# Optimization experiments

Measured on AMD Instinct MI355X. Metric: run time of the kernel, lower is better.

## Reference

```python
import jax, jax.numpy as jnp
import numpy as np

DIM = 1024      # main_dim
HEADS = 16      # attn_num
HEAD = DIM // HEADS
S = 1024        # seq len per half
BH = 1          # batch per half (x_input batch = 2*BH)
PE = 16; FE = 16      # experts per group
PD = 512; FD = 512    # expert hidden dims
DS = 2048             # shared_expert_dim
K = 4                 # top_k routed experts
EPS = 1e-5
THETA = 10000.0
SCALE_P = 1.0; SCALE_F = 1.0


def rmsnorm(x, w, eps=EPS):
    return x * jax.lax.rsqrt(jnp.mean(x * x, -1, keepdims=True) + eps) * w


def rope(x, theta=THETA):
    # x: [b, h, s, a]; matches RotaryEmb: y1 = x1*cos + x2*sin, y2 = -x1*sin + x2*cos
    a = x.shape[-1]; s = x.shape[2]
    inv = (1.0 / theta) ** (jnp.arange(0, a, 2, dtype=jnp.float32) / a)
    fr = jnp.arange(s, dtype=jnp.float32)[:, None] * inv[None, :]   # [s, a//2]
    cos, sin = jnp.cos(fr), jnp.sin(fr)
    x1, x2 = jnp.split(x, 2, -1)
    return jnp.concatenate([x1 * cos + x2 * sin, -x1 * sin + x2 * cos], -1)


def moe(xt, block, idx, sc):
    # xt: [T, d]; block: [3, E, d, f] (gate/up/down SwiGLU); idx, sc: [T, K]
    g = jnp.einsum('td,edf->tef', xt, block[0])
    u = jnp.einsum('td,edf->tef', xt, block[1])
    h = jax.nn.silu(g) * u
    out_all = jnp.einsum('tef,edf->ted', h, block[2])        # per-expert outputs
    sel = jnp.take_along_axis(out_all, idx[:, :, None], 1)   # [T, K, d]
    return jnp.sum(sel * sc[:, :, None], 1)


def setup_inputs():
    key = jax.random.key(0)
    ks = jax.random.split(key, 16)
    w = 0.02  # param scale for numerical sanity
    d = {}
    d['x_input'] = jax.random.normal(ks[0], (2 * BH, S, DIM), jnp.float32)
    d['p_indices'] = jax.random.randint(ks[1], (BH * S, K), 0, PE)
    d['p_values'] = jax.random.normal(ks[2], (BH * S, K), jnp.float32)
    d['f_indices'] = jax.random.randint(ks[3], (BH * S, K), 0, FE)
    d['f_values'] = jax.random.normal(ks[4], (BH * S, K), jnp.float32)
    d['attn_norm_w'] = jnp.ones((DIM,), jnp.float32)
    d['ffn_norm_w'] = jnp.ones((DIM,), jnp.float32)
    d['W_attn'] = jax.random.normal(ks[5], (DIM, 3 * DIM), jnp.float32) * w
    d['W_attn_o'] = jax.random.normal(ks[6], (DIM, DIM), jnp.float32) * w
    d['ffn_up_w'] = jax.random.normal(ks[7], (DIM, 2 * DS), jnp.float32) * w
    d['ffn_down_w'] = jax.random.normal(ks[8], (DS, DIM), jnp.float32) * w
    d['p_ffn_experts'] = jax.random.normal(ks[9], (3, PE, DIM, PD), jnp.float32) * w
    d['f_ffn_experts'] = jax.random.normal(ks[10], (3, FE, DIM, FD), jnp.float32) * w
    d['p_token_keys'] = jax.random.normal(ks[11], (DIM, PE), jnp.float32) * w
    d['f_token_keys'] = jax.random.normal(ks[12], (DIM, FE), jnp.float32) * w
    d['p_router_bias'] = jnp.zeros((PE,), jnp.float32)
    d['f_router_bias'] = jnp.zeros((FE,), jnp.float32)
    return d


def reference(x_input, p_indices, p_values, f_indices, f_values,
              attn_norm_w, ffn_norm_w, W_attn, W_attn_o, ffn_up_w, ffn_down_w,
              p_ffn_experts, f_ffn_experts, p_token_keys, f_token_keys,
              p_router_bias, f_router_bias):
    B2, s, dim = x_input.shape
    b = B2 // 2
    # attention block
    x = rmsnorm(x_input, attn_norm_w)
    xq, xk, xv = jnp.split(x @ W_attn, 3, -1)
    heads = lambda t: t.reshape(B2, s, HEADS, HEAD).transpose(0, 2, 1, 3)
    xq, xk, xv = heads(xq), heads(xk), heads(xv)
    xq, xk = rope(xq), rope(xk)
    # dual interleave: '(c b) h s a -> b h (s c) a', c=2
    il = lambda t: t.reshape(2, b, HEADS, s, HEAD).transpose(1, 2, 3, 0, 4).reshape(b, HEADS, 2 * s, HEAD)
    q, k, v = il(xq), il(xk), il(xv)
    scores = jnp.einsum('bhqa,bhka->bhqk', q, k) / jnp.sqrt(jnp.float32(HEAD))
    causal = jnp.tril(jnp.ones((2 * s, 2 * s), bool))
    attn = jax.nn.softmax(jnp.where(causal, scores, -jnp.inf), -1)
    o = jnp.einsum('bhqk,bhka->bhqa', attn, v)
    # de-interleave: 'b h (s c) a -> (c b) s (h a)'
    o = o.reshape(b, HEADS, s, 2, HEAD).transpose(3, 0, 2, 1, 4).reshape(B2, s, dim)
    x_ffn_input = o @ W_attn_o + x_input
    x_ffn = rmsnorm(x_ffn_input, ffn_norm_w)
    p_x = x_ffn[:b].reshape(-1, dim)
    f_x = x_ffn[b:].reshape(-1, dim)
    # router: token keys + bias, sigmoid, normalize
    p_vals = p_values + jnp.take_along_axis(p_x @ p_token_keys, p_indices, -1) + p_router_bias[p_indices]
    f_vals = f_values + jnp.take_along_axis(f_x @ f_token_keys, f_indices, -1) + f_router_bias[f_indices]
    p_sc = jax.nn.sigmoid(p_vals)
    p_sc = p_sc / jnp.sum(p_sc, -1, keepdims=True) * SCALE_P
    f_sc = jax.nn.sigmoid(f_vals)
    f_sc = f_sc / jnp.sum(f_sc, -1, keepdims=True) * SCALE_F
    py = moe(p_x, p_ffn_experts, p_indices, p_sc).reshape(b, s, dim)
    fy = moe(f_x, f_ffn_experts, f_indices, f_sc).reshape(b, s, dim)
    y = jnp.concatenate([py, fy], 0) + x_ffn_input
    # shared expert (SwiGLU)
    x1, x2 = jnp.split(x_ffn @ ffn_up_w, 2, -1)
    y = y + (jax.nn.silu(x1) * x2) @ ffn_down_w
    return y
```

## Files before the change

### kernel.cpp

```cpp
#include <hip/hip_runtime.h>


#define T_TOT   2048
#define DMODEL  1024
#define NHEADS  16
#define NEXP    16
#define FDIM    512
#define DSH     2048
#define NPAIR   8192

typedef __attribute__((ext_vector_type(4))) float          f32x4;
typedef __attribute__((ext_vector_type(8))) short          s16x8;
typedef __attribute__((ext_vector_type(8))) unsigned short u16x8;
typedef __attribute__((ext_vector_type(2))) unsigned int   u32x2;

__device__ __forceinline__ float sigm(float x) { return 1.0f / (1.0f + __expf(-x)); }

__device__ __forceinline__ unsigned short bf16r(float f) {
    union { float f; unsigned int u; } v; v.f = f;
    unsigned int r = v.u + 0x7fffu + ((v.u >> 16) & 1u);
    return (unsigned short)(r >> 16);
}

__device__ __forceinline__ unsigned int cvtpk(float lo, float hi) {
    unsigned int r;
    asm("v_cvt_pk_bf16_f32 %0, %1, %2" : "=v"(r) : "v"(lo), "v"(hi));
    return r;
}

__device__ __forceinline__ float ubf(unsigned short u) {
    union { unsigned int i; float f; } v; v.i = (unsigned int)u << 16; return v.f;
}

__device__ __forceinline__ int pair2tok(int p) {
    return ((p >> 12) << 10) + ((p & 4095) >> 2);
}

template<int NI>
__device__ __forceinline__ void tile_mma(
        const unsigned short (*Asb)[40], const unsigned short (*Bsb)[40],
        int wm, int wn, int lr, int lk, f32x4 (&acc)[4][NI]) {
    s16x8 af[4], bfr[NI];
    #pragma unroll
    for (int mi = 0; mi < 4; ++mi)
        af[mi] = *(const s16x8*)&Asb[wm + mi * 16 + lr][lk];
    #pragma unroll
    for (int ni = 0; ni < NI; ++ni)
        bfr[ni] = *(const s16x8*)&Bsb[wn + ni * 16 + lr][lk];
    #pragma unroll
    for (int mi = 0; mi < 4; ++mi)
        #pragma unroll
        for (int ni = 0; ni < NI; ++ni)
            acc[mi][ni] = __builtin_amdgcn_mfma_f32_16x16x32_bf16(
                              af[mi], bfr[ni], acc[mi][ni], 0, 0, 0);
}

__device__ __forceinline__ void gu_mma(
        const unsigned short (*Asb)[40], const unsigned short (*Bg)[40],
        const unsigned short (*Bu)[40], int wm, int wn, int lr, int lk,
        f32x4 (&ag)[4][2], f32x4 (&au)[4][2]) {
    s16x8 af[4], bg[2], bu[2];
    #pragma unroll
    for (int mi = 0; mi < 4; ++mi)
        af[mi] = *(const s16x8*)&Asb[wm + mi * 16 + lr][lk];
    #pragma unroll
    for (int ni = 0; ni < 2; ++ni) {
        bg[ni] = *(const s16x8*)&Bg[wn + ni * 16 + lr][lk];
        bu[ni] = *(const s16x8*)&Bu[wn + ni * 16 + lr][lk];
    }
    #pragma unroll
    for (int mi = 0; mi < 4; ++mi)
        #pragma unroll
        for (int ni = 0; ni < 2; ++ni) {
            ag[mi][ni] = __builtin_amdgcn_mfma_f32_16x16x32_bf16(
                             af[mi], bg[ni], ag[mi][ni], 0, 0, 0);
            au[mi][ni] = __builtin_amdgcn_mfma_f32_16x16x32_bf16(
                             af[mi], bu[ni], au[mi][ni], 0, 0, 0);
        }
}

__global__ void rmsnorm_kernel(const float* __restrict__ x,
                               const float* __restrict__ w,
                               unsigned short* __restrict__ out) {
    int t = blockIdx.x, tid = threadIdx.x;
    float4 xv = *(const float4*)(x + (size_t)t * DMODEL + tid * 4);
    __shared__ float rb[256];
    rb[tid] = xv.x*xv.x + xv.y*xv.y + xv.z*xv.z + xv.w*xv.w;
    __syncthreads();
    for (int s = 128; s > 0; s >>= 1) { if (tid < s) rb[tid] += rb[tid+s]; __syncthreads(); }
    float scale = rsqrtf(rb[0] * (1.0f/1024.0f) + 1e-5f);
    float4 wv = *(const float4*)(w + tid * 4);
    u32x2 pv;
    pv.x = cvtpk(xv.x * scale * wv.x, xv.y * scale * wv.y);
    pv.y = cvtpk(xv.z * scale * wv.z, xv.w * scale * wv.w);
    *(u32x2*)(out + (size_t)t * DMODEL + tid * 4) = pv;
}

__global__ void rope_kernel(unsigned short* __restrict__ qkv) {
    int t = blockIdx.x, tid = threadIdx.x;
    int s = t & 1023;
    unsigned short* row = qkv + (size_t)t * 3072;
    for (int pp = tid; pp < 512; pp += 256) {
        int h = pp >> 5, i = pp & 31;
        float fr = (float)s * exp2f(-0.41524101186092028f * (float)i);
        float sn, cs;
        sincosf(fr, &sn, &cs);
        int o1 = (h << 6) + i, o2 = o1 + 32;
        float x1 = ubf(row[o1]), x2 = ubf(row[o2]);
        row[o1] = bf16r(x1 * cs + x2 * sn);
        row[o2] = bf16r(x2 * cs - x1 * sn);
        x1 = ubf(row[1024 + o1]); x2 = ubf(row[1024 + o2]);
        row[1024 + o1] = bf16r(x1 * cs + x2 * sn);
        row[1024 + o2] = bf16r(x2 * cs - x1 * sn);
    }
}

__global__ __launch_bounds__(256) void attn_mfma_kernel(
        const unsigned short* __restrict__ qkv,
        unsigned short* __restrict__ attn_out) {
    int qt = blockIdx.x, h = blockIdx.y;
    __shared__ alignas(16) unsigned short Qs[64][72];
    __shared__ alignas(16) unsigned short Ks[64][72];
    __shared__ alignas(16) unsigned short Vt[64][72];
    __shared__ alignas(16) unsigned short Ps[4][16][72];
    int tid = threadIdx.x;
    int w = tid >> 6, lane = tid & 63;
    int lr = lane & 15, lkg = lane >> 4, lk = lkg << 3;
    int kr = tid >> 3, kc = (tid & 7) << 3;

    #pragma unroll
    for (int i = 0; i < 2; ++i) {
        int rr = kr + 32 * i;
        int p = qt * 64 + rr;
        int t = ((p & 1) << 10) + (p >> 1);
        u16x8 q = *(const u16x8*)(qkv + (size_t)t * 3072 + (h << 6) + kc);
        unsigned int* dst = (unsigned int*)&Qs[rr][kc];
        dst[0] = cvtpk(ubf(q[0]) * 0.125f, ubf(q[1]) * 0.125f);
        dst[1] = cvtpk(ubf(q[2]) * 0.125f, ubf(q[3]) * 0.125f);
        dst[2] = cvtpk(ubf(q[4]) * 0.125f, ubf(q[5]) * 0.125f);
        dst[3] = cvtpk(ubf(q[6]) * 0.125f, ubf(q[7]) * 0.125f);
    }
    u16x8 pkv[2], pvv[2];
    #pragma unroll
    for (int i = 0; i < 2; ++i) {
        int rr = kr + 32 * i;
        int t = ((rr & 1) << 10) + (rr >> 1);
        const unsigned short* b = qkv + (size_t)t * 3072 + (h << 6) + kc;
        pkv[i] = *(const u16x8*)(b + 1024);
        pvv[i] = *(const u16x8*)(b + 2048);
    }
    __syncthreads();
    s16x8 qa0 = *(const s16x8*)&Qs[(w << 4) + lr][lk];
    s16x8 qa1 = *(const s16x8*)&Qs[(w << 4) + lr][32 + lk];

    float m[4], l[4];
    f32x4 oacc[4];
    #pragma unroll
    for (int r = 0; r < 4; ++r) { m[r] = -1e30f; l[r] = 0.0f; }
    #pragma unroll
    for (int df = 0; df < 4; ++df) oacc[df] = (f32x4)0.0f;

    int qrow_base = qt * 64 + w * 16 + lkg * 4;

    for (int kb = 0; kb <= qt; ++kb) {
        __syncthreads();
        u16x8 ck[2], cv[2];
        #pragma unroll
        for (int i = 0; i < 2; ++i) { ck[i] = pkv[i]; cv[i] = pvv[i]; }
        if (kb + 1 <= qt) {
            #pragma unroll
            for (int i = 0; i < 2; ++i) {
                int rr = kr + 32 * i;
                int p = (kb + 1) * 64 + rr;
                int t = ((p & 1) << 10) + (p >> 1);
                const unsigned short* b = qkv + (size_t)t * 3072 + (h << 6) + kc;
                pkv[i] = *(const u16x8*)(b + 1024);
                pvv[i] = *(const u16x8*)(b + 2048);
            }
        }
        #pragma unroll
        for (int i = 0; i < 2; ++i) {
            int rr = kr + 32 * i;
            *(u16x8*)&Ks[rr][kc] = ck[i];
            #pragma unroll
            for (int j = 0; j < 8; ++j) {
                int vrow = kc + j;
                int sw = ((vrow >> 3) & 7) << 3;
                Vt[vrow][rr ^ sw] = cv[i][j];
            }
        }
        __syncthreads();

        f32x4 s[4];
        #pragma unroll
        for (int nf = 0; nf < 4; ++nf) {
            s16x8 b0 = *(const s16x8*)&Ks[nf * 16 + lr][lk];
            s16x8 b1 = *(const s16x8*)&Ks[nf * 16 + lr][32 + lk];
            f32x4 z = (f32x4)0.0f;
            z = __builtin_amdgcn_mfma_f32_16x16x32_bf16(qa0, b0, z, 0, 0, 0);
            z = __builtin_amdgcn_mfma_f32_16x16x32_bf16(qa1, b1, z, 0, 0, 0);
            s[nf] = z;
        }
        if (kb == qt) {
            #pragma unroll
            for (int nf = 0; nf < 4; ++nf) {
                int kcol = kb * 64 + nf * 16 + lr;
                #pragma unroll
                for (int r = 0; r < 4; ++r)
                    if (kcol > qrow_base + r) s[nf][r] = -1e30f;
            }
        }
        float mloc[4];
        #pragma unroll
        for (int r = 0; r < 4; ++r)
            mloc[r] = fmaxf(fmaxf(s[0][r], s[1][r]), fmaxf(s[2][r], s[3][r]));
        #pragma unroll
        for (int r = 0; r < 4; ++r) {
            mloc[r] = fmaxf(mloc[r], __shfl_xor(mloc[r], 1));
            mloc[r] = fmaxf(mloc[r], __shfl_xor(mloc[r], 2));
            mloc[r] = fmaxf(mloc[r], __shfl_xor(mloc[r], 4));
            mloc[r] = fmaxf(mloc[r], __shfl_xor(mloc[r], 8));
        }
        float alpha[4], psum[4];
        #pragma unroll
        for (int r = 0; r < 4; ++r) {
            float mnew = fmaxf(m[r], mloc[r]);
            alpha[r] = __expf(m[r] - mnew);
            m[r] = mnew;
            psum[r] = 0.0f;
        }
        #pragma unroll
        for (int nf = 0; nf < 4; ++nf)
            #pragma unroll
            for (int r = 0; r < 4; ++r) {
                float pv2 = __expf(s[nf][r] - m[r]);
                s[nf][r] = pv2;
                psum[r] += pv2;
            }
        #pragma unroll
        for (int r = 0; r < 4; ++r) {
            psum[r] += __shfl_xor(psum[r], 1);
            psum[r] += __shfl_xor(psum[r], 2);
            psum[r] += __shfl_xor(psum[r], 4);
            psum[r] += __shfl_xor(psum[r], 8);
            l[r] = l[r] * alpha[r] + psum[r];
        }
        #pragma unroll
        for (int nf = 0; nf < 4; ++nf)
            #pragma unroll
            for (int r = 0; r < 4; ++r)
                Ps[w][lkg * 4 + r][nf * 16 + lr] = bf16r(s[nf][r]);
        #pragma unroll
        for (int df = 0; df < 4; ++df)
            #pragma unroll
            for (int r = 0; r < 4; ++r)
                oacc[df][r] *= alpha[r];
        s16x8 pa0 = *(const s16x8*)&Ps[w][lr][lk];
        s16x8 pa1 = *(const s16x8*)&Ps[w][lr][32 + lk];
        #pragma unroll
        for (int df = 0; df < 4; ++df) {
            int vr = df * 16 + lr;
            int sw = ((vr >> 3) & 7) << 3;
            s16x8 v0 = *(const s16x8*)&Vt[vr][lk ^ sw];
            s16x8 v1 = *(const s16x8*)&Vt[vr][(32 + lk) ^ sw];
            oacc[df] = __builtin_amdgcn_mfma_f32_16x16x32_bf16(pa0, v0, oacc[df], 0, 0, 0);
            oacc[df] = __builtin_amdgcn_mfma_f32_16x16x32_bf16(pa1, v1, oacc[df], 0, 0, 0);
        }
    }

    float invl[4];
    #pragma unroll
    for (int r = 0; r < 4; ++r) invl[r] = 1.0f / l[r];
    #pragma unroll
    for (int r = 0; r < 4; ++r) {
        int qrow = qrow_base + r;
        int t = ((qrow & 1) << 10) + (qrow >> 1);
        unsigned short* op = attn_out + (size_t)t * 1024 + (h << 6) + lr;
        #pragma unroll
        for (int df = 0; df < 4; ++df)
            op[df * 16] = bf16r(oacc[df][r] * invl[r]);
    }
}

__global__ void router_kernel(const unsigned short* __restrict__ xffn,
        const float* __restrict__ p_keys, const float* __restrict__ f_keys,
        const int* __restrict__ p_idx, const int* __restrict__ f_idx,
        const float* __restrict__ p_val, const float* __restrict__ f_val,
        const float* __restrict__ p_bias, const float* __restrict__ f_bias,
        float* __restrict__ sc) {
    int tl = blockIdx.x, hf = blockIdx.y;
    int t = hf * 1024 + tl;
    const float* keys = hf ? f_keys : p_keys;
    const int* idx    = hf ? f_idx  : p_idx;
    const float* val  = hf ? f_val  : p_val;
    const float* bias = hf ? f_bias : p_bias;
    int tid = threadIdx.x;
    float acc[16];
    #pragma unroll
    for (int e = 0; e < 16; ++e) acc[e] = 0.0f;
    const unsigned short* x = xffn + (size_t)t * DMODEL;
    for (int d = tid; d < 1024; d += 256) {
        float xd = ubf(x[d]);
        const float* kr = keys + d * 16;
        #pragma unroll
        for (int e4 = 0; e4 < 4; ++e4) {
            float4 kv = *(const float4*)(kr + e4 * 4);
            acc[e4*4+0] += xd * kv.x;
            acc[e4*4+1] += xd * kv.y;
            acc[e4*4+2] += xd * kv.z;
            acc[e4*4+3] += xd * kv.w;
        }
    }
    #pragma unroll
    for (int e = 0; e < 16; ++e) {
        float v = acc[e];
        v += __shfl_down(v, 32); v += __shfl_down(v, 16); v += __shfl_down(v, 8);
        v += __shfl_down(v, 4);  v += __shfl_down(v, 2);  v += __shfl_down(v, 1);
        acc[e] = v;
    }
    __shared__ float part[4][16];
    __shared__ float logit[16];
    __shared__ float sg[4];
    int wave = tid >> 6, ln = tid & 63;
    if (ln == 0) {
        #pragma unroll
        for (int e = 0; e < 16; ++e) part[wave][e] = acc[e];
    }
    __syncthreads();
    if (tid < 16) logit[tid] = part[0][tid] + part[1][tid] + part[2][tid] + part[3][tid];
    __syncthreads();
    if (tid < 4) {
        int ii = idx[tl * 4 + tid];
        float v = val[tl * 4 + tid] + logit[ii] + bias[ii];
        sg[tid] = 1.0f / (1.0f + expf(-v));
    }
    __syncthreads();
    if (tid < 4) {
        float ssum = sg[0] + sg[1] + sg[2] + sg[3];
        sc[t * 4 + tid] = sg[tid] / ssum;
    }
}

__global__ __launch_bounds__(1024) void buckets_kernel(
        const int* __restrict__ p_idx, const int* __restrict__ f_idx,
        int* __restrict__ counts, int* __restrict__ offsets,
        int* __restrict__ pair_p) {
    __shared__ int lcnt[32], loff[32], lcur[32];
    int tid = threadIdx.x;
    if (tid < 32) { lcnt[tid] = 0; lcur[tid] = 0; }
    __syncthreads();
    for (int p = tid; p < NPAIR; p += 1024) {
        int hf = p >> 12, rem = p & 4095;
        int e = (hf ? f_idx : p_idx)[rem];
        atomicAdd(&lcnt[(hf << 4) + e], 1);
    }
    __syncthreads();
    if (tid == 0) {
        int o = 0;
        for (int b = 0; b < 32; ++b) { loff[b] = o; o += lcnt[b]; }
    }
    __syncthreads();
    for (int p = tid; p < NPAIR; p += 1024) {
        int hf = p >> 12, rem = p & 4095;
        int e = (hf ? f_idx : p_idx)[rem];
        int b = (hf << 4) + e;
        int pos = atomicAdd(&lcur[b], 1);
        pair_p[loff[b] + pos] = p;
    }
    if (tid < 32) { counts[tid] = lcnt[tid]; offsets[tid] = loff[tid]; }
}

template<int MODE, int BN2, int OUTBF>
__global__ __launch_bounds__(256) void mfma_gemm(
        const unsigned short* __restrict__ A, const float* __restrict__ B,
        void* __restrict__ Cv, const float* __restrict__ resid,
        int M, int N, int K) {
    constexpr int NI = BN2 / 32;
    __shared__ alignas(16) unsigned short As[2][128][40];
    __shared__ alignas(16) unsigned short Bs[2][BN2][40];
    int tid = threadIdx.x;
    int m0 = blockIdx.y * 128, n0 = blockIdx.x * BN2;
    int w = tid >> 6, lane = tid & 63;
    int wm = (w >> 1) * 64, wn = (w & 1) * (BN2 / 2);
    int lr = lane & 15, lk = (lane >> 4) << 3;
    int ar = tid >> 2, ac = (tid & 3) << 3;
    int bn = (tid >> 3) << 2, bk = (tid & 7) << 2;
    bool bact = true;
    if (BN2 == 64) bact = (tid < 128);
    const unsigned short* Ap0 = A + (size_t)(m0 + ar) * K + ac;
    const unsigned short* Ap1 = Ap0 + (size_t)64 * K;
    const float* Bp = B + (size_t)bk * N + n0 + bn;

    f32x4 acc[4][NI] = {};
    u16x8 aA0, aA1, aB0, aB1;
    f32x4 bA[4], bB[4];

#define GM_LOAD(A0, A1, BV, KK) do {                                      \
        A0 = *(const u16x8*)(Ap0 + (KK));                                 \
        A1 = *(const u16x8*)(Ap1 + (KK));                                 \
        if (bact) {                                                       \
            const float* bp_ = Bp + (size_t)(KK) * N;                     \
            _Pragma("unroll")                                             \
            for (int j = 0; j < 4; ++j)                                   \
                BV[j] = *(const f32x4*)(bp_ + (size_t)j * N);             \
        }                                                                 \
    } while (0)

#define GM_WRITE(BUF, A0, A1, BV) do {                                    \
        *(u16x8*)&As[BUF][ar][ac] = A0;                                   \
        *(u16x8*)&As[BUF][ar + 64][ac] = A1;                              \
        if (bact) {                                                       \
            _Pragma("unroll")                                             \
            for (int jj = 0; jj < 4; ++jj) {                              \
                u32x2 pv_;                                                \
                pv_.x = cvtpk(BV[0][jj], BV[1][jj]);                      \
                pv_.y = cvtpk(BV[2][jj], BV[3][jj]);                      \
                *(u32x2*)&Bs[BUF][bn + jj][bk] = pv_;                     \
            }                                                             \
        }                                                                 \
    } while (0)

    GM_LOAD(aA0, aA1, bA, 0);
    GM_LOAD(aB0, aB1, bB, 32);
    GM_WRITE(0, aA0, aA1, bA);
    __syncthreads();
    for (int k0 = 0; k0 < K; k0 += 64) {
        if (k0 + 64 < K) GM_LOAD(aA0, aA1, bA, k0 + 64);
        tile_mma<NI>(As[0], Bs[0], wm, wn, lr, lk, acc);
        GM_WRITE(1, aB0, aB1, bB);
        __syncthreads();
        if (k0 + 96 < K) GM_LOAD(aB0, aB1, bB, k0 + 96);
        tile_mma<NI>(As[1], Bs[1], wm, wn, lr, lk, acc);
        if (k0 + 64 < K) GM_WRITE(0, aA0, aA1, bA);
        __syncthreads();
    }
#undef GM_LOAD
#undef GM_WRITE

    #pragma unroll
    for (int mi = 0; mi < 4; ++mi)
        #pragma unroll
        for (int r = 0; r < 4; ++r) {
            int row = m0 + wm + mi * 16 + ((lane >> 4) << 2) + r;
            size_t rb = (size_t)row * N + n0 + wn + lr;
            #pragma unroll
            for (int ni = 0; ni < NI; ++ni) {
                size_t off = rb + ni * 16;
                float v = acc[mi][ni][r];
                if constexpr (OUTBF) {
                    ((unsigned short*)Cv)[off] = bf16r(v);
                } else {
                    float* Cf = (float*)Cv;
                    if (MODE == 1) v += Cf[off];
                    if (MODE == 2) v += resid[off];
                    Cf[off] = v;
                }
            }
        }
}

template<int MOE>
__global__ __launch_bounds__(256) void mfma_gateup(
        const unsigned short* __restrict__ X, const float* __restrict__ Wp,
        const float* __restrict__ Wf, const int* __restrict__ pair_p,
        const int* __restrict__ counts, const int* __restrict__ offsets,
        unsigned short* __restrict__ Hout) {
    __shared__ alignas(16) unsigned short As[2][128][40];
    __shared__ alignas(16) unsigned short Bsg[2][64][40];
    __shared__ alignas(16) unsigned short Bsu[2][64][40];
    __shared__ int toks[128];
    int tid = threadIdx.x;
    int rem = 128, slot0 = 0, m0 = 0, n0, ldb;
    const float *Wg, *Wu;
    if (MOE) {
        int bucket = blockIdx.y;
        int cnt = counts[bucket];
        int tile0 = blockIdx.x * 128;
        if (tile0 >= cnt) return;
        n0 = blockIdx.z * 64;
        int e = bucket & 15;
        const float* base = (bucket >> 4) ? Wf : Wp;
        Wg = base + (size_t)e * (DMODEL * FDIM) + n0;
        Wu = base + (size_t)(NEXP + e) * (DMODEL * FDIM) + n0;
        ldb = FDIM;
        slot0 = offsets[bucket] + tile0;
        rem = cnt - tile0;
        if (tid < 128)
            toks[tid] = (tid < rem) ? pair2tok(pair_p[slot0 + tid]) : 0;
    } else {
        m0 = blockIdx.y * 128;
        n0 = blockIdx.x * 64;
        Wg = Wp + n0;
        Wu = Wp + DSH + n0;
        ldb = 2 * DSH;
    }
    int w = tid >> 6, lane = tid & 63;
    int wm = (w >> 1) * 64, wn = (w & 1) * 32;
    int lr = lane & 15, lk = (lane >> 4) << 3;
    int ar = tid >> 2, ac = (tid & 3) << 3;
    int t2 = tid & 127, wq = tid >> 7;
    int bn = (t2 >> 3) << 2, bk = (t2 & 7) << 2;
    const float* bsrc = wq ? Wu : Wg;
    if (MOE) __syncthreads();
    const unsigned short *Xp0, *Xp1;
    {
        int x0 = MOE ? toks[ar] : (m0 + ar);
        int x1 = MOE ? toks[ar + 64] : (m0 + ar + 64);
        Xp0 = X + (size_t)x0 * DMODEL + ac;
        Xp1 = X + (size_t)x1 * DMODEL + ac;
    }
    const float* Bp = bsrc + (size_t)bk * ldb + bn;
    f32x4 ag[4][2] = {}, au[4][2] = {};
    u16x8 aA0, aA1, aB0, aB1;
    f32x4 bA[4], bB[4];

#define GU_LOAD(A0, A1, BV, KK) do {                                      \
        A0 = *(const u16x8*)(Xp0 + (KK));                                 \
        A1 = *(const u16x8*)(Xp1 + (KK));                                 \
        {                                                                 \
            const float* bp_ = Bp + (size_t)(KK) * ldb;                   \
            _Pragma("unroll")                                             \
            for (int j = 0; j < 4; ++j)                                   \
                BV[j] = *(const f32x4*)(bp_ + (size_t)j * ldb);           \
        }                                                                 \
    } while (0)

#define GU_WRITE(BUF, A0, A1, BV) do {                                    \
        *(u16x8*)&As[BUF][ar][ac] = A0;                                   \
        *(u16x8*)&As[BUF][ar + 64][ac] = A1;                              \
        {                                                                 \
            unsigned short (*bl_)[40] = wq ? Bsu[BUF] : Bsg[BUF];         \
            _Pragma("unroll")                                             \
            for (int jj = 0; jj < 4; ++jj) {                              \
                u32x2 pv_;                                                \
                pv_.x = cvtpk(BV[0][jj], BV[1][jj]);                      \
                pv_.y = cvtpk(BV[2][jj], BV[3][jj]);                      \
                *(u32x2*)&bl_[bn + jj][bk] = pv_;                         \
            }                                                             \
        }                                                                 \
    } while (0)

    GU_LOAD(aA0, aA1, bA, 0);
    GU_LOAD(aB0, aB1, bB, 32);
    GU_WRITE(0, aA0, aA1, bA);
    __syncthreads();
    for (int k0 = 0; k0 < DMODEL; k0 += 64) {
        if (k0 + 64 < DMODEL) GU_LOAD(aA0, aA1, bA, k0 + 64);
        gu_mma(As[0], Bsg[0], Bsu[0], wm, wn, lr, lk, ag, au);
        GU_WRITE(1, aB0, aB1, bB);
        __syncthreads();
        if (k0 + 96 < DMODEL) GU_LOAD(aB0, aB1, bB, k0 + 96);
        gu_mma(As[1], Bsg[1], Bsu[1], wm, wn, lr, lk, ag, au);
        if (k0 + 64 < DMODEL) GU_WRITE(0, aA0, aA1, bA);
        __syncthreads();
    }
#undef GU_LOAD
#undef GU_WRITE

    #pragma unroll
    for (int mi = 0; mi < 4; ++mi)
        #pragma unroll
        for (int r = 0; r < 4; ++r) {
            int rloc = wm + mi * 16 + ((lane >> 4) << 2) + r;
            if (MOE && rloc >= rem) continue;
            size_t rowb = MOE ? (size_t)(slot0 + rloc) * FDIM
                              : (size_t)(m0 + rloc) * DSH;
            #pragma unroll
            for (int ni = 0; ni < 2; ++ni) {
                float g = ag[mi][ni][r], u = au[mi][ni][r];
                Hout[rowb + n0 + wn + ni * 16 + lr] = bf16r(g * sigm(g) * u);
            }
        }
}

__global__ __launch_bounds__(256) void mfma_moe_down(
        const unsigned short* __restrict__ h_pairs,
        const float* __restrict__ p_experts, const float* __restrict__ f_experts,
        const int* __restrict__ pair_p, const int* __restrict__ counts,
        const int* __restrict__ offsets, const float* __restrict__ sc,
        float* __restrict__ y) {
    __shared__ alignas(16) unsigned short As[2][128][40];
    __shared__ alignas(16) unsigned short Bs[2][128][40];
    __shared__ int   tokd[128];
    __shared__ float scd[128];
    int tid = threadIdx.x;
    int bucket = blockIdx.y;
    int cnt = counts[bucket];
    int tile0 = blockIdx.x * 128;
    if (tile0 >= cnt) return;
    int d0 = blockIdx.z * 128;
    int e = bucket & 15;
    const float* base = (bucket >> 4) ? f_experts : p_experts;
    const float* Wd = base + (size_t)(2 * NEXP + e) * (DMODEL * FDIM);
    int slot0 = offsets[bucket] + tile0;
    int rem = cnt - tile0;
    if (tid < 128) {
        int ok = tid < rem;
        int pr = ok ? pair_p[slot0 + tid] : 0;
        tokd[tid] = pair2tok(pr);
        scd[tid]  = ok ? sc[pr] : 0.0f;
    }
    int w = tid >> 6, lane = tid & 63;
    int wm = (w >> 1) * 64, wn = (w & 1) * 64;
    int lr = lane & 15, lk = (lane >> 4) << 3;
    int ar = tid >> 2, ac = (tid & 3) << 3;
    int br = tid >> 3, bc = (tid & 7) << 2;
    const unsigned short* Ap0 = h_pairs + (size_t)(slot0 + ar) * FDIM + ac;
    const unsigned short* Ap1 = Ap0 + (size_t)64 * FDIM;
    const float* Bp0 = Wd + (size_t)(d0 + br) * FDIM + bc;
    f32x4 acc[4][4] = {};
    u16x8 aA0, aA1, aB0, aB1;
    f32x4 bA[4], bB[4];

#define MD_LOAD(A0, A1, BV, KK) do {                                      \
        A0 = *(const u16x8*)(Ap0 + (KK));                                 \
        A1 = *(const u16x8*)(Ap1 + (KK));                                 \
        _Pragma("unroll")                                                 \
        for (int i = 0; i < 4; ++i)                                       \
            BV[i] = *(const f32x4*)(Bp0 + (size_t)(32 * i) * FDIM + (KK));\
    } while (0)

#define MD_WRITE(BUF, A0, A1, BV) do {                                    \
        *(u16x8*)&As[BUF][ar][ac] = A0;                                   \
        *(u16x8*)&As[BUF][ar + 64][ac] = A1;                              \
        _Pragma("unroll")                                                 \
        for (int i = 0; i < 4; ++i) {                                     \
            u32x2 pv_;                                                    \
            pv_.x = cvtpk(BV[i][0], BV[i][1]);                            \
            pv_.y = cvtpk(BV[i][2], BV[i][3]);                            \
            *(u32x2*)&Bs[BUF][br + 32 * i][bc] = pv_;                     \
        }                                                                 \
    } while (0)

    MD_LOAD(aA0, aA1, bA, 0);
    MD_LOAD(aB0, aB1, bB, 32);
    MD_WRITE(0, aA0, aA1, bA);
    __syncthreads();
    for (int k0 = 0; k0 < FDIM; k0 += 64) {
        if (k0 + 64 < FDIM) MD_LOAD(aA0, aA1, bA, k0 + 64);
        tile_mma<4>(As[0], Bs[0], wm, wn, lr, lk, acc);
        MD_WRITE(1, aB0, aB1, bB);
        __syncthreads();
        if (k0 + 96 < FDIM) MD_LOAD(aB0, aB1, bB, k0 + 96);
        tile_mma<4>(As[1], Bs[1], wm, wn, lr, lk, acc);
        if (k0 + 64 < FDIM) MD_WRITE(0, aA0, aA1, bA);
        __syncthreads();
    }
#undef MD_LOAD
#undef MD_WRITE

    #pragma unroll
    for (int mi = 0; mi < 4; ++mi)
        #pragma unroll
        for (int r = 0; r < 4; ++r) {
            int rloc = wm + mi * 16 + ((lane >> 4) << 2) + r;
            if (rloc < rem) {
                int   t = tokd[rloc];
                float s = scd[rloc];
                float* yp = y + (size_t)t * DMODEL + d0 + wn + lr;
                #pragma unroll
                for (int ni = 0; ni < 4; ++ni)
                    atomicAdd(yp + ni * 16, s * acc[mi][ni][r]);
            }
        }
}

extern "C" void kernel_launch(void* const* d_in, const int* in_sizes, int n_in,
                              void* d_out, int out_size, void* d_ws, size_t ws_size,
                              hipStream_t stream) {
    const float* x_input  = (const float*)d_in[0];
    const int*   p_idx    = (const int*)d_in[1];
    const float* p_val    = (const float*)d_in[2];
    const int*   f_idx    = (const int*)d_in[3];
    const float* f_val    = (const float*)d_in[4];
    const float* attn_w   = (const float*)d_in[5];
    const float* ffn_w    = (const float*)d_in[6];
    const float* W_attn   = (const float*)d_in[7];
    const float* W_attn_o = (const float*)d_in[8];
    const float* ffn_up   = (const float*)d_in[9];
    const float* ffn_down = (const float*)d_in[10];
    const float* p_exp    = (const float*)d_in[11];
    const float* f_exp    = (const float*)d_in[12];
    const float* p_keys   = (const float*)d_in[13];
    const float* f_keys   = (const float*)d_in[14];
    const float* p_bias   = (const float*)d_in[15];
    const float* f_bias   = (const float*)d_in[16];
    float* y32 = (float*)d_out;
    (void)in_sizes; (void)n_in; (void)out_size; (void)ws_size;

    float* ws = (float*)d_ws;
    unsigned short* xnormh    = (unsigned short*)ws;
    unsigned short* attn_outh = (unsigned short*)ws;
    unsigned short* qkvh      = (unsigned short*)(ws + 2097152);
    unsigned short* h_pairsh  = (unsigned short*)(ws + 2097152);
    unsigned short* hsh       = (unsigned short*)(ws + 2097152);
    float* x_ffn_in  = ws + 8388608;
    unsigned short* x_ffnh = (unsigned short*)(ws + 10485760);
    float* sc        = ws + 12582912;
    int*   counts    = (int*)(ws + 12591104);
    int*   offsets   = counts + 32;
    int*   pair_p    = offsets + 32;

    rmsnorm_kernel<<<T_TOT, 256, 0, stream>>>(x_input, attn_w, xnormh);
    mfma_gemm<0, 128, 1><<<dim3(24, 16), 256, 0, stream>>>(xnormh, W_attn, qkvh,
                                                           nullptr, T_TOT, 3072, 1024);
    rope_kernel<<<T_TOT, 256, 0, stream>>>(qkvh);
    attn_mfma_kernel<<<dim3(32, NHEADS), 256, 0, stream>>>(qkvh, attn_outh);
    mfma_gemm<2, 64, 0><<<dim3(16, 16), 256, 0, stream>>>(attn_outh, W_attn_o,
                                                          x_ffn_in, x_input,
                                                          T_TOT, 1024, 1024);
    rmsnorm_kernel<<<T_TOT, 256, 0, stream>>>(x_ffn_in, ffn_w, x_ffnh);
    router_kernel<<<dim3(1024, 2), 256, 0, stream>>>(x_ffnh, p_keys, f_keys,
                                                     p_idx, f_idx, p_val, f_val,
                                                     p_bias, f_bias, sc);
    buckets_kernel<<<1, 1024, 0, stream>>>(p_idx, f_idx, counts, offsets, pair_p);
    mfma_gateup<1><<<dim3(4, 32, 8), 256, 0, stream>>>(x_ffnh, p_exp, f_exp,
                                                       pair_p, counts, offsets,
                                                       h_pairsh);
    hipMemcpyAsync(y32, x_ffn_in, (size_t)T_TOT * DMODEL * sizeof(float),
                   hipMemcpyDeviceToDevice, stream);
    mfma_moe_down<<<dim3(4, 32, 8), 256, 0, stream>>>(h_pairsh, p_exp, f_exp,
                                                      pair_p, counts, offsets,
                                                      sc, y32);
    mfma_gateup<0><<<dim3(32, 16), 256, 0, stream>>>(x_ffnh, ffn_up, nullptr,
                                                     nullptr, nullptr, nullptr, hsh);
    mfma_gemm<1, 64, 0><<<dim3(16, 16), 256, 0, stream>>>(hsh, ffn_down, y32,
                                                          nullptr, T_TOT, 1024, 2048);
}
```

Before: 628.2 us.

## Split MoE gate/up into separate projection tiles plus standalone SiLU kernel

The fused MoE gate/up kernel, which computed both gate and up with 64-wide N tiles, is replaced by a projection kernel that computes either gate or up with 128-wide tiles over a flattened 1D grid. Its bf16 outputs go to temporary buffers, and a separate elementwise kernel applies SiLU(g)*u. The MoE down kernel switches to the same flattened grid, which puts a bucket's tiles next to each other in dispatch order. The change adds an extra global round-trip of the gate and up intermediates and an extra launch, in exchange for larger MFMA tiles and possibly better occupancy and scheduling.

Result: no change. 620.1 us (-1.3%).

```diff
diff --git a/kernel.cpp b/kernel.cpp
--- a/kernel.cpp
+++ b/kernel.cpp
@@ -459,41 +459,17 @@
         }
 }
 
-template<int MOE>
-__global__ __launch_bounds__(256) void mfma_gateup(
-        const unsigned short* __restrict__ X, const float* __restrict__ Wp,
-        const float* __restrict__ Wf, const int* __restrict__ pair_p,
-        const int* __restrict__ counts, const int* __restrict__ offsets,
+__global__ __launch_bounds__(256) void mfma_gateup_dense(
+        const unsigned short* __restrict__ X, const float* __restrict__ W1,
         unsigned short* __restrict__ Hout) {
     __shared__ alignas(16) unsigned short As[2][128][40];
     __shared__ alignas(16) unsigned short Bsg[2][64][40];
     __shared__ alignas(16) unsigned short Bsu[2][64][40];
-    __shared__ int toks[128];
     int tid = threadIdx.x;
-    int rem = 128, slot0 = 0, m0 = 0, n0, ldb;
-    const float *Wg, *Wu;
-    if (MOE) {
-        int bucket = blockIdx.y;
-        int cnt = counts[bucket];
-        int tile0 = blockIdx.x * 128;
-        if (tile0 >= cnt) return;
-        n0 = blockIdx.z * 64;
-        int e = bucket & 15;
-        const float* base = (bucket >> 4) ? Wf : Wp;
-        Wg = base + (size_t)e * (DMODEL * FDIM) + n0;
-        Wu = base + (size_t)(NEXP + e) * (DMODEL * FDIM) + n0;
-        ldb = FDIM;
-        slot0 = offsets[bucket] + tile0;
-        rem = cnt - tile0;
-        if (tid < 128)
-            toks[tid] = (tid < rem) ? pair2tok(pair_p[slot0 + tid]) : 0;
-    } else {
-        m0 = blockIdx.y * 128;
-        n0 = blockIdx.x * 64;
-        Wg = Wp + n0;
-        Wu = Wp + DSH + n0;
-        ldb = 2 * DSH;
-    }
+    int m0 = blockIdx.y * 128, n0 = blockIdx.x * 64;
+    const float* Wg = W1 + n0;
+    const float* Wu = W1 + DSH + n0;
+    int ldb = 2 * DSH;
     int w = tid >> 6, lane = tid & 63;
     int wm = (w >> 1) * 64, wn = (w & 1) * 32;
     int lr = lane & 15, lk = (lane >> 4) << 3;
@@ -501,14 +477,8 @@
     int t2 = tid & 127, wq = tid >> 7;
     int bn = (t2 >> 3) << 2, bk = (t2 & 7) << 2;
     const float* bsrc = wq ? Wu : Wg;
-    if (MOE) __syncthreads();
-    const unsigned short *Xp0, *Xp1;
-    {
-        int x0 = MOE ? toks[ar] : (m0 + ar);
-        int x1 = MOE ? toks[ar + 64] : (m0 + ar + 64);
-        Xp0 = X + (size_t)x0 * DMODEL + ac;
-        Xp1 = X + (size_t)x1 * DMODEL + ac;
-    }
+    const unsigned short* Xp0 = X + (size_t)(m0 + ar) * DMODEL + ac;
+    const unsigned short* Xp1 = Xp0 + (size_t)64 * DMODEL;
     const float* Bp = bsrc + (size_t)bk * ldb + bn;
     f32x4 ag[4][2] = {}, au[4][2] = {};
     u16x8 aA0, aA1, aB0, aB1;
@@ -562,15 +532,119 @@
         #pragma unroll
         for (int r = 0; r < 4; ++r) {
             int rloc = wm + mi * 16 + ((lane >> 4) << 2) + r;
-            if (MOE && rloc >= rem) continue;
-            size_t rowb = MOE ? (size_t)(slot0 + rloc) * FDIM
-                              : (size_t)(m0 + rloc) * DSH;
+            size_t rowb = (size_t)(m0 + rloc) * DSH;
             #pragma unroll
             for (int ni = 0; ni < 2; ++ni) {
                 float g = ag[mi][ni][r], u = au[mi][ni][r];
                 Hout[rowb + n0 + wn + ni * 16 + lr] = bf16r(g * sigm(g) * u);
             }
         }
+}
+
+__global__ __launch_bounds__(256) void moe_proj_kernel(
+        const unsigned short* __restrict__ X,
+        const float* __restrict__ p_experts, const float* __restrict__ f_experts,
+        const int* __restrict__ pair_p, const int* __restrict__ counts,
+        const int* __restrict__ offsets,
+        unsigned short* __restrict__ gtmp, unsigned short* __restrict__ utmp) {
+    __shared__ alignas(16) unsigned short As[2][128][40];
+    __shared__ alignas(16) unsigned short Bs[2][128][40];
+    __shared__ int toks[128];
+    int i = blockIdx.x;
+    int bucket = i >> 5, xt = (i >> 3) & 3, z = i & 7;
+    int cnt = counts[bucket];
+    int tile0 = xt * 128;
+    if (tile0 >= cnt) return;
+    int mat = z & 1, f0 = (z >> 1) * 128;
+    int e = bucket & 15;
+    const float* basep = (bucket >> 4) ? f_experts : p_experts;
+    const float* W = basep + (size_t)((mat ? NEXP : 0) + e) * (DMODEL * FDIM) + f0;
+    unsigned short* out = mat ? utmp : gtmp;
+    int slot0 = offsets[bucket] + tile0;
+    int rem = cnt - tile0;
+    int tid = threadIdx.x;
+    if (tid < 128)
+        toks[tid] = (tid < rem) ? pair2tok(pair_p[slot0 + tid]) : 0;
+    __syncthreads();
+    int w = tid >> 6, lane = tid & 63;
+    int wm = (w >> 1) * 64, wn = (w & 1) * 64;
+    int lr = lane & 15, lk = (lane >> 4) << 3;
+    int ar = tid >> 2, ac = (tid & 3) << 3;
+    int bn = (tid >> 3) << 2, bk = (tid & 7) << 2;
+    const unsigned short* Xp0 = X + (size_t)toks[ar] * DMODEL + ac;
+    const unsigned short* Xp1 = X + (size_t)toks[ar + 64] * DMODEL + ac;
+    const float* Bp = W + (size_t)bk * FDIM + bn;
+    f32x4 acc[4][4] = {};
+    u16x8 aA0, aA1, aB0, aB1;
+    f32x4 bA[4], bB[4];
+
+#define PR_LOAD(A0, A1, BV, KK) do {                                      \
+        A0 = *(const u16x8*)(Xp0 + (KK));                                 \
+        A1 = *(const u16x8*)(Xp1 + (KK));                                 \
+        {                                                                 \
+            const float* bp_ = Bp + (size_t)(KK) * FDIM;                  \
+            _Pragma("unroll")                                             \
+            for (int j = 0; j < 4; ++j)                                   \
+                BV[j] = *(const f32x4*)(bp_ + (size_t)j * FDIM);          \
+        }                                                                 \
+    } while (0)
+
+#define PR_WRITE(BUF, A0, A1, BV) do {                                    \
+        *(u16x8*)&As[BUF][ar][ac] = A0;                                   \
+        *(u16x8*)&As[BUF][ar + 64][ac] = A1;                              \
+        _Pragma("unroll")                                                 \
+        for (int jj = 0; jj < 4; ++jj) {                                  \
+            u32x2 pv_;                                                    \
+            pv_.x = cvtpk(BV[0][jj], BV[1][jj]);                          \
+            pv_.y = cvtpk(BV[2][jj], BV[3][jj]);                          \
+            *(u32x2*)&Bs[BUF][bn + jj][bk] = pv_;                         \
+        }                                                                 \
+    } while (0)
+
+    PR_LOAD(aA0, aA1, bA, 0);
+    PR_LOAD(aB0, aB1, bB, 32);
+    PR_WRITE(0, aA0, aA1, bA);
+    __syncthreads();
+    for (int k0 = 0; k0 < DMODEL; k0 += 64) {
+        if (k0 + 64 < DMODEL) PR_LOAD(aA0, aA1, bA, k0 + 64);
+        tile_mma<4>(As[0], Bs[0], wm, wn, lr, lk, acc);
+        PR_WRITE(1, aB0, aB1, bB);
+        __syncthreads();
+        if (k0 + 96 < DMODEL) PR_LOAD(aB0, aB1, bB, k0 + 96);
+        tile_mma<4>(As[1], Bs[1], wm, wn, lr, lk, acc);
+        if (k0 + 64 < DMODEL) PR_WRITE(0, aA0, aA1, bA);
+        __syncthreads();
+    }
+#undef PR_LOAD
+#undef PR_WRITE
+
+    #pragma unroll
+    for (int mi = 0; mi < 4; ++mi)
+        #pragma unroll
+        for (int r = 0; r < 4; ++r) {
+            int rloc = wm + mi * 16 + ((lane >> 4) << 2) + r;
+            if (rloc < rem) {
+                size_t rowb = (size_t)(slot0 + rloc) * FDIM + f0 + wn + lr;
+                #pragma unroll
+                for (int ni = 0; ni < 4; ++ni)
+                    out[rowb + ni * 16] = bf16r(acc[mi][ni][r]);
+            }
+        }
+}
+
+__global__ void moe_silu_kernel(const unsigned short* __restrict__ g,
+                                const unsigned short* __restrict__ u,
+                                unsigned short* __restrict__ h) {
+    size_t i = ((size_t)blockIdx.x * 256 + threadIdx.x) * 8;
+    u16x8 gv = *(const u16x8*)(g + i);
+    u16x8 uv = *(const u16x8*)(u + i);
+    u16x8 o;
+    #pragma unroll
+    for (int j = 0; j < 8; ++j) {
+        float gf = ubf(gv[j]);
+        o[j] = bf16r(gf * sigm(gf) * ubf(uv[j]));
+    }
+    *(u16x8*)(h + i) = o;
 }
 
 __global__ __launch_bounds__(256) void mfma_moe_down(
@@ -583,17 +657,18 @@
     __shared__ alignas(16) unsigned short Bs[2][128][40];
     __shared__ int   tokd[128];
     __shared__ float scd[128];
-    int tid = threadIdx.x;
-    int bucket = blockIdx.y;
+    int i = blockIdx.x;
+    int bucket = i >> 5, xt = (i >> 3) & 3, z = i & 7;
     int cnt = counts[bucket];
-    int tile0 = blockIdx.x * 128;
+    int tile0 = xt * 128;
     if (tile0 >= cnt) return;
-    int d0 = blockIdx.z * 128;
+    int d0 = z * 128;
     int e = bucket & 15;
     const float* base = (bucket >> 4) ? f_experts : p_experts;
     const float* Wd = base + (size_t)(2 * NEXP + e) * (DMODEL * FDIM);
     int slot0 = offsets[bucket] + tile0;
     int rem = cnt - tile0;
+    int tid = threadIdx.x;
     if (tid < 128) {
         int ok = tid < rem;
         int pr = ok ? pair_p[slot0 + tid] : 0;
@@ -616,22 +691,23 @@
         A0 = *(const u16x8*)(Ap0 + (KK));                                 \
         A1 = *(const u16x8*)(Ap1 + (KK));                                 \
         _Pragma("unroll")                                                 \
-        for (int i = 0; i < 4; ++i)                                       \
-            BV[i] = *(const f32x4*)(Bp0 + (size_t)(32 * i) * FDIM + (KK));\
+        for (int i2 = 0; i2 < 4; ++i2)                                    \
+            BV[i2] = *(const f32x4*)(Bp0 + (size_t)(32 * i2) * FDIM + (KK));\
     } while (0)
 
 #define MD_WRITE(BUF, A0, A1, BV) do {                                    \
         *(u16x8*)&As[BUF][ar][ac] = A0;                                   \
         *(u16x8*)&As[BUF][ar + 64][ac] = A1;                              \
         _Pragma("unroll")                                                 \
-        for (int i = 0; i < 4; ++i) {                                     \
+        for (int i2 = 0; i2 < 4; ++i2) {                                  \
             u32x2 pv_;                                                    \
-            pv_.x = cvtpk(BV[i][0], BV[i][1]);                            \
-            pv_.y = cvtpk(BV[i][2], BV[i][3]);                            \
-            *(u32x2*)&Bs[BUF][br + 32 * i][bc] = pv_;                     \
+            pv_.x = cvtpk(BV[i2][0], BV[i2][1]);                          \
+            pv_.y = cvtpk(BV[i2][2], BV[i2][3]);                          \
+            *(u32x2*)&Bs[BUF][br + 32 * i2][bc] = pv_;                    \
         }                                                                 \
     } while (0)
 
+    __syncthreads();
     MD_LOAD(aA0, aA1, bA, 0);
     MD_LOAD(aB0, aB1, bB, 32);
     MD_WRITE(0, aA0, aA1, bA);
@@ -691,8 +767,10 @@
     float* ws = (float*)d_ws;
     unsigned short* xnormh    = (unsigned short*)ws;
     unsigned short* attn_outh = (unsigned short*)ws;
+    unsigned short* gtmp      = (unsigned short*)ws;
     unsigned short* qkvh      = (unsigned short*)(ws + 2097152);
-    unsigned short* h_pairsh  = (unsigned short*)(ws + 2097152);
+    unsigned short* utmp      = (unsigned short*)(ws + 2097152);
+    unsigned short* h_pairsh  = (unsigned short*)(ws + 4194304);
     unsigned short* hsh       = (unsigned short*)(ws + 2097152);
     float* x_ffn_in  = ws + 8388608;
     unsigned short* x_ffnh = (unsigned short*)(ws + 10485760);
@@ -714,16 +792,16 @@
                                                      p_idx, f_idx, p_val, f_val,
                                                      p_bias, f_bias, sc);
     buckets_kernel<<<1, 1024, 0, stream>>>(p_idx, f_idx, counts, offsets, pair_p);
-    mfma_gateup<1><<<dim3(4, 32, 8), 256, 0, stream>>>(x_ffnh, p_exp, f_exp,
-                                                       pair_p, counts, offsets,
-                                                       h_pairsh);
+    moe_proj_kernel<<<1024, 256, 0, stream>>>(x_ffnh, p_exp, f_exp,
+                                              pair_p, counts, offsets,
+                                              gtmp, utmp);
+    moe_silu_kernel<<<2048, 256, 0, stream>>>(gtmp, utmp, h_pairsh);
     hipMemcpyAsync(y32, x_ffn_in, (size_t)T_TOT * DMODEL * sizeof(float),
                    hipMemcpyDeviceToDevice, stream);
-    mfma_moe_down<<<dim3(4, 32, 8), 256, 0, stream>>>(h_pairsh, p_exp, f_exp,
-                                                      pair_p, counts, offsets,
-                                                      sc, y32);
-    mfma_gateup<0><<<dim3(32, 16), 256, 0, stream>>>(x_ffnh, ffn_up, nullptr,
-                                                     nullptr, nullptr, nullptr, hsh);
+    mfma_moe_down<<<1024, 256, 0, stream>>>(h_pairsh, p_exp, f_exp,
+                                            pair_p, counts, offsets,
+                                            sc, y32);
+    mfma_gateup_dense<<<dim3(32, 16), 256, 0, stream>>>(x_ffnh, ffn_up, hsh);
     mfma_gemm<1, 64, 0><<<dim3(16, 16), 256, 0, stream>>>(hsh, ffn_down, y32,
                                                           nullptr, T_TOT, 1024, 2048);
 }
```
